# Optimization experiments

Hardware: AMD Instinct MI355X
Metric: run time of the kernel (lower is better)

## Reference

```python
import jax, jax.numpy as jnp
import numpy as np
from math import ceil, sqrt

# Inner module: Linear(2048,4096)+ReLU, Linear(4096,4096)+ReLU, Linear(4096,2048)
D_IN, D_H, D_OUT = 2048, 4096, 2048
BATCH = 4096
# named_modules() order: each Linear yields weight then bias; ReLU skipped
SHAPES = [(D_H, D_IN), (D_H,), (D_H, D_H), (D_H,), (D_OUT, D_H), (D_OUT,)]
NUM_P = sum(int(np.prod(s)) for s in SHAPES)  # 33_566_720
SIZE_N = ceil(sqrt(NUM_P))                    # 5794
SIZE_M = ceil(1.0 * SIZE_N / 2)               # 2897 (compress = 1.0)


def setup_inputs() -> dict:
    key = jax.random.key(0)
    k1, k2, k3 = jax.random.split(key, 3)
    k = sqrt(12) / 2 * SIZE_M ** (-0.25)  # norm_V init bound
    V1 = jax.random.uniform(k1, (SIZE_N, SIZE_M), jnp.float32, -k, k)
    V2 = jax.random.uniform(k2, (SIZE_M, SIZE_N), jnp.float32, -k, k)
    x = jax.random.normal(k3, (BATCH, D_IN), jnp.float32)
    return {"x": x, "V1": V1, "V2": V2}


def _unpack(Vf):
    # scatter-copy: contiguous slices of flattened V -> weights/biases in traversal order
    params, i = [], 0
    for s in SHAPES:
        n = int(np.prod(s))
        params.append(Vf[i:i + n].reshape(s))
        i += n
    return params


def reference(x, V1, V2):
    # WandBtoV: low-rank reconstruction then per-element copy into weights (fused here)
    Vf = (V1 @ V2).reshape(-1)  # [SIZE_N*SIZE_N]; only first NUM_P elements used
    W1, b1, W2, b2, W3, b3 = _unpack(Vf)
    h = jax.nn.relu(x @ W1.T + b1)   # [B, D_H]
    h = jax.nn.relu(h @ W2.T + b2)   # [B, D_H]
    return h @ W3.T + b3             # [B, D_OUT]
```

## Files before the change

kernel.cpp:

```cpp
#include <hip/hip_runtime.h>
#include <stdint.h>

typedef __attribute__((ext_vector_type(8)))  __bf16 bf16x8;
typedef __attribute__((ext_vector_type(16))) float  f32x16;
typedef unsigned short u16;
typedef __attribute__((ext_vector_type(8))) unsigned short u16x8;

#define GLOBAL_AS __attribute__((address_space(1)))
#define LDS_AS    __attribute__((address_space(3)))

__device__ __forceinline__ void load_lds16(const void* g, void* l) {
    __builtin_amdgcn_global_load_lds((const GLOBAL_AS void*)g, (LDS_AS void*)l, 16, 0, 0);
}

__device__ __forceinline__ u16 f2bf(float f) {
    union { float f; uint32_t u; } v; v.f = f;
    uint32_t r = v.u + 0x7FFFu + ((v.u >> 16) & 1u);
    return (u16)(r >> 16);
}
__device__ __forceinline__ float b2f(u16 b) {
    union { uint32_t u; float f; } v; v.u = ((uint32_t)b) << 16;
    return v.f;
}

__global__ void k_conv_pad(const float* __restrict__ in, u16* __restrict__ out,
                           int rIn, int cIn, int cOut, int total8) {
    int idx = blockIdx.x * blockDim.x + threadIdx.x;
    if (idx >= total8) return;
    int c8n = cOut >> 3;
    int r  = idx / c8n;
    int c0 = (idx - r * c8n) << 3;
    u16x8 o;
#pragma unroll
    for (int j = 0; j < 8; ++j) {
        int c = c0 + j;
        o[j] = (r < rIn && c < cIn) ? f2bf(in[(size_t)r * cIn + c]) : (u16)0;
    }
    *(u16x8*)(out + (size_t)r * cOut + c0) = o;
}

__global__ void k_transpose_conv(const float* __restrict__ in, u16* __restrict__ out,
                                 int kIn, int nIn, int kOut) {
    __shared__ float tile[32][33];
    int k0 = blockIdx.x * 32, n0 = blockIdx.y * 32;
    int tx = threadIdx.x, ty = threadIdx.y;
#pragma unroll
    for (int i = 0; i < 4; ++i) {
        int k = k0 + ty + i * 8, n = n0 + tx;
        tile[ty + i * 8][tx] = (k < kIn && n < nIn) ? in[(size_t)k * nIn + n] : 0.f;
    }
    __syncthreads();
#pragma unroll
    for (int i = 0; i < 4; ++i) {
        int n = n0 + ty + i * 8, k = k0 + tx;
        out[(size_t)n * kOut + k] = f2bf(tile[tx][ty + i * 8]);
    }
}

template <int MODE>
__global__ __launch_bounds__(256, 4) void k_gemm_bt(
    const u16* __restrict__ A, const u16* __restrict__ B,
    const u16* __restrict__ bias, void* __restrict__ Cv,
    int K, int ldc, int mReal, int nReal) {
    (void)bias;
    __shared__ __align__(16) char lds[32768];
    char* As = lds;
    char* Bs = lds + 16384;

    const int tid  = threadIdx.x;
    const int w    = tid >> 6, lane = tid & 63;
    const int l31  = lane & 31, hi = lane >> 5;
    const int wm   = (w & 1) * 64, wn = (w >> 1) * 64;
    const int bm   = blockIdx.y * 128, bn = blockIdx.x * 128;

    const int srcRow = tid >> 3;
    const int srcCol = (tid & 7) ^ (srcRow & 7);
    const u16* aSrc = A + (size_t)(bm + srcRow) * K + (srcCol << 3);
    const u16* bSrc = B + (size_t)(bn + srcRow) * K + (srcCol << 3);
    char* aDst = As + ((tid & ~63) << 4);
    char* bDst = Bs + ((tid & ~63) << 4);

    const int aRow0 = (wm + l31) * 128;
    const int aRow1 = (wm + 32 + l31) * 128;
    const int bRow0 = (wn + l31) * 128;
    const int bRow1 = (wn + 32 + l31) * 128;

    f32x16 acc[2][2];
#pragma unroll
    for (int i = 0; i < 2; ++i)
#pragma unroll
        for (int j = 0; j < 2; ++j) acc[i][j] = (f32x16)(0.f);

    for (int k0 = 0; k0 < K; k0 += 64) {
#pragma unroll
        for (int t = 0; t < 4; ++t) {
            load_lds16(aSrc + (size_t)(t * 32) * K, aDst + t * 4096);
            load_lds16(bSrc + (size_t)(t * 32) * K, bDst + t * 4096);
        }
        aSrc += 64; bSrc += 64;
        __syncthreads();
#pragma unroll
        for (int ks = 0; ks < 4; ++ks) {
            const int swz = (((ks * 2 + hi) ^ (l31 & 7)) << 4);
            bf16x8 af[2], bfr[2];
            af[0]  = *(const bf16x8*)(As + aRow0 + swz);
            af[1]  = *(const bf16x8*)(As + aRow1 + swz);
            bfr[0] = *(const bf16x8*)(Bs + bRow0 + swz);
            bfr[1] = *(const bf16x8*)(Bs + bRow1 + swz);
#pragma unroll
            for (int mi = 0; mi < 2; ++mi)
#pragma unroll
                for (int ni = 0; ni < 2; ++ni)
                    acc[mi][ni] = __builtin_amdgcn_mfma_f32_32x32x16_bf16(
                        af[mi], bfr[ni], acc[mi][ni], 0, 0, 0);
        }
        __syncthreads();
    }

    float bv[2];
    if (MODE >= 1) {
#pragma unroll
        for (int ni = 0; ni < 2; ++ni) bv[ni] = b2f(bias[bn + wn + ni * 32 + l31]);
    }
#pragma unroll
    for (int mi = 0; mi < 2; ++mi) {
#pragma unroll
        for (int reg = 0; reg < 16; ++reg) {
            int row = bm + wm + mi * 32 + (reg & 3) + 8 * (reg >> 2) + 4 * hi;
#pragma unroll
            for (int ni = 0; ni < 2; ++ni) {
                int col = bn + wn + ni * 32 + l31;
                float v = acc[mi][ni][reg];
                if (MODE == 0) {
                    if (row < mReal && col < nReal)
                        ((u16*)Cv)[(size_t)row * ldc + col] = f2bf(v);
                } else if (MODE == 1) {
                    v += bv[ni];
                    v = v > 0.f ? v : 0.f;
                    ((u16*)Cv)[(size_t)row * ldc + col] = f2bf(v);
                } else {
                    ((float*)Cv)[(size_t)row * ldc + col] = v + bv[ni];
                }
            }
        }
    }
}


#define BARRIER() do { asm volatile("" ::: "memory"); \
                       __builtin_amdgcn_s_barrier(); \
                       asm volatile("" ::: "memory"); } while (0)
#define LGKM0()   do { asm volatile("s_waitcnt lgkmcnt(0)" ::: "memory"); \
                       __builtin_amdgcn_sched_barrier(0); } while (0)
#define VMCNT0()  do { asm volatile("s_waitcnt vmcnt(0)" ::: "memory"); \
                       __builtin_amdgcn_sched_barrier(0); } while (0)

#define STAGE8(bb, koff) do { \
    _Pragma("unroll") for (int t = 0; t < 4; ++t) \
        load_lds16(aS + (koff) + (size_t)(t * 64) * K, (bb) + wOff + t * 8192); \
    _Pragma("unroll") for (int t = 0; t < 4; ++t) \
        load_lds16(bS + (koff) + (size_t)(t * 64) * K, (bb) + 32768 + wOff + t * 8192); \
} while (0)

#define RD6(bb, p, FA, FB) do { \
    FA[0] = *(const bf16x8*)((bb) + aB +     0 + (p) * 1024); \
    FA[1] = *(const bf16x8*)((bb) + aB +  4096 + (p) * 1024); \
    FA[2] = *(const bf16x8*)((bb) + aB +  8192 + (p) * 1024); \
    FA[3] = *(const bf16x8*)((bb) + aB + 12288 + (p) * 1024); \
    FB[0] = *(const bf16x8*)((bb) + bB +     0 + (p) * 1024); \
    FB[1] = *(const bf16x8*)((bb) + bB +  4096 + (p) * 1024); \
} while (0)

#define MM8(FA, FB) do { \
    __builtin_amdgcn_s_setprio(1); \
    acc[0][0] = __builtin_amdgcn_mfma_f32_32x32x16_bf16(FA[0], FB[0], acc[0][0], 0, 0, 0); \
    acc[1][0] = __builtin_amdgcn_mfma_f32_32x32x16_bf16(FA[1], FB[0], acc[1][0], 0, 0, 0); \
    acc[2][0] = __builtin_amdgcn_mfma_f32_32x32x16_bf16(FA[2], FB[0], acc[2][0], 0, 0, 0); \
    acc[3][0] = __builtin_amdgcn_mfma_f32_32x32x16_bf16(FA[3], FB[0], acc[3][0], 0, 0, 0); \
    acc[0][1] = __builtin_amdgcn_mfma_f32_32x32x16_bf16(FA[0], FB[1], acc[0][1], 0, 0, 0); \
    acc[1][1] = __builtin_amdgcn_mfma_f32_32x32x16_bf16(FA[1], FB[1], acc[1][1], 0, 0, 0); \
    acc[2][1] = __builtin_amdgcn_mfma_f32_32x32x16_bf16(FA[2], FB[1], acc[2][1], 0, 0, 0); \
    acc[3][1] = __builtin_amdgcn_mfma_f32_32x32x16_bf16(FA[3], FB[1], acc[3][1], 0, 0, 0); \
    __builtin_amdgcn_s_setprio(0); \
} while (0)

template <int MODE>
__global__ __launch_bounds__(512, 2) void k_gemm256(
    const u16* __restrict__ A, const u16* __restrict__ B,
    const u16* __restrict__ bias, void* __restrict__ Cv,
    int K, int ldc, int mReal, int nReal, int gx, int nTiles) {
    __shared__ __align__(16) char lds[131072];

    const int tid  = threadIdx.x;
    const int w    = tid >> 6, lane = tid & 63;
    const int l31  = lane & 31, hi = lane >> 5;
    const int wr   = w & 1, wc = w >> 1;

    const int cpx = (int)gridDim.x >> 3;
    const int wg0 = ((int)blockIdx.x & 7) * cpx + ((int)blockIdx.x >> 3);

    char* const buf0 = lds;
    char* const buf1 = lds + 65536;

    const int srcRowT = ((w >> 2) * 32) + l31;
    const int kOffT   = (w & 3) * 16 + (hi << 3);
    const int wOff    = w * 1024;

    const int aB = wr * 16384 + lane * 16;
    const int bB = 32768 + wc * 8192 + lane * 16;

    const int nIt = K >> 7;

    for (int v = wg0; v < nTiles; v += (int)gridDim.x) {
        const int bm = (v / gx) * 256;
        const int bn = (v % gx) * 256;
        const u16* const aS = A + (size_t)(bm + srcRowT) * K + kOffT;
        const u16* const bS = B + (size_t)(bn + srcRowT) * K + kOffT;

        f32x16 acc[4][2];
#pragma unroll
        for (int i = 0; i < 4; ++i)
#pragma unroll
            for (int j = 0; j < 2; ++j) acc[i][j] = (f32x16)(0.f);

        bf16x8 xa[4], xb[2], ya[4], yb[2];

        STAGE8(buf0, 0);
        VMCNT0();
        BARRIER();

        size_t ko = 0;
#pragma unroll 1
        for (int it = 0; it < nIt; ++it) {
            STAGE8(buf1, ko + 64);
            RD6(buf0, 0, xa, xb);
            RD6(buf0, 1, ya, yb);
            MM8(xa, xb);
            RD6(buf0, 2, xa, xb);
            MM8(ya, yb);
            RD6(buf0, 3, ya, yb);
            MM8(xa, xb);
            LGKM0(); VMCNT0(); BARRIER();
            if (it + 1 < nIt) { STAGE8(buf0, ko + 128); }
            MM8(ya, yb);
            RD6(buf1, 0, xa, xb);
            RD6(buf1, 1, ya, yb);
            MM8(xa, xb);
            RD6(buf1, 2, xa, xb);
            MM8(ya, yb);
            RD6(buf1, 3, ya, yb);
            MM8(xa, xb);
            LGKM0(); VMCNT0(); BARRIER();
            MM8(ya, yb);
            ko += 128;
        }

        float bv[2];
        if (MODE >= 1) {
#pragma unroll
            for (int ni = 0; ni < 2; ++ni) bv[ni] = b2f(bias[bn + wc * 64 + ni * 32 + l31]);
        }
#pragma unroll
        for (int mi = 0; mi < 4; ++mi) {
#pragma unroll
            for (int reg = 0; reg < 16; ++reg) {
                const int row = bm + wr * 128 + mi * 32 + (reg & 3) + 8 * (reg >> 2) + 4 * hi;
#pragma unroll
                for (int ni = 0; ni < 2; ++ni) {
                    const int col = bn + wc * 64 + ni * 32 + l31;
                    float vv = acc[mi][ni][reg];
                    if (MODE == 0) {
                        if (row < mReal && col < nReal)
                            ((u16*)Cv)[(size_t)row * ldc + col] = f2bf(vv);
                    } else if (MODE == 1) {
                        vv += bv[ni];
                        vv = vv > 0.f ? vv : 0.f;
                        ((u16*)Cv)[(size_t)row * ldc + col] = f2bf(vv);
                    } else {
                        ((float*)Cv)[(size_t)row * ldc + col] = vv + bv[ni];
                    }
                }
            }
        }
    }
}

extern "C" void kernel_launch(void* const* d_in, const int* in_sizes, int n_in,
                              void* d_out, int out_size, void* d_ws, size_t ws_size,
                              hipStream_t stream) {
    (void)in_sizes; (void)n_in; (void)out_size; (void)ws_size;
    const float* x  = (const float*)d_in[0];
    const float* V1 = (const float*)d_in[1];
    const float* V2 = (const float*)d_in[2];

    char* ws = (char*)d_ws;
    u16* Vf   = (u16*)(ws);
    u16* V1b  = (u16*)(ws + 67141120);
    u16* V2bT = (u16*)(ws + 67141120 + 34668544);
    u16* Xb   = (u16*)(ws + 67141120 + 2 * 34668544);
    u16* H1   = V1b;
    u16* H2   = V2bT;

    k_conv_pad<<<8464, 256, 0, stream>>>(V1, V1b, 5794, 2897, 2944, 5888 * 2944 / 8);
    k_transpose_conv<<<dim3(92, 184), dim3(32, 8), 0, stream>>>(V2, V2bT, 2897, 5794, 2944);
    k_conv_pad<<<4096, 256, 0, stream>>>(x, Xb, 4096, 2048, 2048, 4096 * 2048 / 8);

    k_gemm256<0><<<512, 512, 0, stream>>>(V1b, V2bT, nullptr, Vf,
                                          2944, 5794, 5794, 5794, 23, 529);
    k_gemm256<1><<<256, 512, 0, stream>>>(Xb, Vf + 0, Vf + 8388608, H1,
                                          2048, 4096, 4096, 4096, 16, 256);
    k_gemm256<1><<<256, 512, 0, stream>>>(H1, Vf + 8392704, Vf + 25169920, H2,
                                          4096, 4096, 4096, 4096, 16, 256);
    k_gemm_bt<2><<<dim3(16, 32), 256, 0, stream>>>(H2, Vf + 25174016, Vf + 33562624, d_out,
                                                   4096, 2048, 4096, 2048);
}
```

Baseline: 852.9 us.

## Replace 256x256 persistent GEMM with 256x128 non-persistent tiles and swizzled LDS

The 512-thread persistent 256x256-tile GEMM is replaced by a 256-thread kernel computing 256x128 tiles, one tile per workgroup, with a K-step of 64 and a smaller double-buffered LDS footprint. LDS rows are stored with an XOR swizzle on 16-byte chunks to avoid bank conflicts. Block-to-XCD remapping now handles grid sizes that are not a multiple of 8. The aim is more workgroups, better occupancy and fewer LDS conflicts, at the cost of less operand reuse per tile and more global traffic.

```diff
diff --git a/kernel.cpp b/kernel.cpp
--- a/kernel.cpp
+++ b/kernel.cpp
@@ -155,20 +155,21 @@
 #define VMCNT0()  do { asm volatile("s_waitcnt vmcnt(0)" ::: "memory"); \
                        __builtin_amdgcn_sched_barrier(0); } while (0)
 
-#define STAGE8(bb, koff) do { \
+#define STAGE6(bb, koff) do { \
     _Pragma("unroll") for (int t = 0; t < 4; ++t) \
-        load_lds16(aS + (koff) + (size_t)(t * 64) * K, (bb) + wOff + t * 8192); \
-    _Pragma("unroll") for (int t = 0; t < 4; ++t) \
-        load_lds16(bS + (koff) + (size_t)(t * 64) * K, (bb) + 32768 + wOff + t * 8192); \
+        load_lds16(aS + (koff) + (size_t)(t * 64) * K, (bb) + t * 4096 + wOff); \
+    _Pragma("unroll") for (int t = 0; t < 2; ++t) \
+        load_lds16(bS + (koff) + (size_t)(t * 64) * K, (bb) + 16384 + t * 4096 + wOff); \
 } while (0)
 
 #define RD6(bb, p, FA, FB) do { \
-    FA[0] = *(const bf16x8*)((bb) + aB +     0 + (p) * 1024); \
-    FA[1] = *(const bf16x8*)((bb) + aB +  4096 + (p) * 1024); \
-    FA[2] = *(const bf16x8*)((bb) + aB +  8192 + (p) * 1024); \
-    FA[3] = *(const bf16x8*)((bb) + aB + 12288 + (p) * 1024); \
-    FB[0] = *(const bf16x8*)((bb) + bB +     0 + (p) * 1024); \
-    FB[1] = *(const bf16x8*)((bb) + bB +  4096 + (p) * 1024); \
+    const int co_ = ch0 ^ ((p) << 5); \
+    FA[0] = *(const bf16x8*)((bb) + aR +    0 + co_); \
+    FA[1] = *(const bf16x8*)((bb) + aR + 2048 + co_); \
+    FA[2] = *(const bf16x8*)((bb) + aR + 4096 + co_); \
+    FA[3] = *(const bf16x8*)((bb) + aR + 6144 + co_); \
+    FB[0] = *(const bf16x8*)((bb) + bR +    0 + co_); \
+    FB[1] = *(const bf16x8*)((bb) + bR + 2048 + co_); \
 } while (0)
 
 #define MM8(FA, FB) do { \
@@ -185,100 +186,92 @@
 } while (0)
 
 template <int MODE>
-__global__ __launch_bounds__(512, 2) void k_gemm256(
+__global__ __launch_bounds__(256, 2) void k_gemm128(
     const u16* __restrict__ A, const u16* __restrict__ B,
     const u16* __restrict__ bias, void* __restrict__ Cv,
-    int K, int ldc, int mReal, int nReal, int gx, int nTiles) {
-    __shared__ __align__(16) char lds[131072];
+    int K, int ldc, int mReal, int nReal, int gx) {
+    __shared__ __align__(16) char lds[49152];
 
     const int tid  = threadIdx.x;
     const int w    = tid >> 6, lane = tid & 63;
     const int l31  = lane & 31, hi = lane >> 5;
     const int wr   = w & 1, wc = w >> 1;
 
-    const int cpx = (int)gridDim.x >> 3;
-    const int wg0 = ((int)blockIdx.x & 7) * cpx + ((int)blockIdx.x >> 3);
+    const int nwg = (int)gridDim.x;
+    const int q   = nwg >> 3, r = nwg & 7;
+    const int xcd = (int)blockIdx.x & 7, lid = (int)blockIdx.x >> 3;
+    const int wg  = (xcd < r ? xcd * (q + 1) : r * (q + 1) + (xcd - r) * q) + lid;
+    const int bm  = (wg / gx) * 256;
+    const int bn  = (wg % gx) * 128;
 
     char* const buf0 = lds;
-    char* const buf1 = lds + 65536;
-
-    const int srcRowT = ((w >> 2) * 32) + l31;
-    const int kOffT   = (w & 3) * 16 + (hi << 3);
-    const int wOff    = w * 1024;
-
-    const int aB = wr * 16384 + lane * 16;
-    const int bB = 32768 + wc * 8192 + lane * 16;
-
-    const int nIt = K >> 7;
-
-    for (int v = wg0; v < nTiles; v += (int)gridDim.x) {
-        const int bm = (v / gx) * 256;
-        const int bn = (v % gx) * 256;
-        const u16* const aS = A + (size_t)(bm + srcRowT) * K + kOffT;
-        const u16* const bS = B + (size_t)(bn + srcRowT) * K + kOffT;
-
-        f32x16 acc[4][2];
-#pragma unroll
-        for (int i = 0; i < 4; ++i)
-#pragma unroll
-            for (int j = 0; j < 2; ++j) acc[i][j] = (f32x16)(0.f);
-
-        bf16x8 xa[4], xb[2], ya[4], yb[2];
-
-        STAGE8(buf0, 0);
-        VMCNT0();
-        BARRIER();
-
-        size_t ko = 0;
+    char* const buf1 = lds + 24576;
+
+    const int srcRow = tid >> 2;
+    const int srcCh  = (tid & 3) ^ ((srcRow >> 1) & 3);
+    const int wOff   = (tid & ~63) << 4;
+
+    const int aR  = (wr * 128 + l31) * 64;
+    const int bR  = 16384 + (wc * 64 + l31) * 64;
+    const int ch0 = ((hi ^ ((l31 >> 1) & 3))) << 4;
+
+    const u16* const aS = A + (size_t)(bm + srcRow) * K + (srcCh << 3);
+    const u16* const bS = B + (size_t)(bn + srcRow) * K + (srcCh << 3);
+
+    f32x16 acc[4][2];
+#pragma unroll
+    for (int i = 0; i < 4; ++i)
+#pragma unroll
+        for (int j = 0; j < 2; ++j) acc[i][j] = (f32x16)(0.f);
+
+    bf16x8 xa[4], xb[2], ya[4], yb[2];
+
+    STAGE6(buf0, 0);
+    VMCNT0();
+    BARRIER();
+
+    const int nIt = K >> 6;
+    size_t ko = 0;
 #pragma unroll 1
-        for (int it = 0; it < nIt; ++it) {
-            STAGE8(buf1, ko + 64);
-            RD6(buf0, 0, xa, xb);
-            RD6(buf0, 1, ya, yb);
-            MM8(xa, xb);
-            RD6(buf0, 2, xa, xb);
-            MM8(ya, yb);
-            RD6(buf0, 3, ya, yb);
-            MM8(xa, xb);
-            LGKM0(); VMCNT0(); BARRIER();
-            if (it + 1 < nIt) { STAGE8(buf0, ko + 128); }
-            MM8(ya, yb);
-            RD6(buf1, 0, xa, xb);
-            RD6(buf1, 1, ya, yb);
-            MM8(xa, xb);
-            RD6(buf1, 2, xa, xb);
-            MM8(ya, yb);
-            RD6(buf1, 3, ya, yb);
-            MM8(xa, xb);
-            LGKM0(); VMCNT0(); BARRIER();
-            MM8(ya, yb);
-            ko += 128;
-        }
-
-        float bv[2];
-        if (MODE >= 1) {
-#pragma unroll
-            for (int ni = 0; ni < 2; ++ni) bv[ni] = b2f(bias[bn + wc * 64 + ni * 32 + l31]);
-        }
-#pragma unroll
-        for (int mi = 0; mi < 4; ++mi) {
-#pragma unroll
-            for (int reg = 0; reg < 16; ++reg) {
-                const int row = bm + wr * 128 + mi * 32 + (reg & 3) + 8 * (reg >> 2) + 4 * hi;
-#pragma unroll
-                for (int ni = 0; ni < 2; ++ni) {
-                    const int col = bn + wc * 64 + ni * 32 + l31;
-                    float vv = acc[mi][ni][reg];
-                    if (MODE == 0) {
-                        if (row < mReal && col < nReal)
-                            ((u16*)Cv)[(size_t)row * ldc + col] = f2bf(vv);
-                    } else if (MODE == 1) {
-                        vv += bv[ni];
-                        vv = vv > 0.f ? vv : 0.f;
+    for (int it = 0; it < nIt; ++it) {
+        STAGE6(buf1, ko + 32);
+        RD6(buf0, 0, xa, xb);
+        RD6(buf0, 1, ya, yb);
+        MM8(xa, xb);
+        LGKM0(); VMCNT0(); BARRIER();
+        if (it + 1 < nIt) { STAGE6(buf0, ko + 64); }
+        MM8(ya, yb);
+        RD6(buf1, 0, xa, xb);
+        RD6(buf1, 1, ya, yb);
+        MM8(xa, xb);
+        LGKM0(); VMCNT0(); BARRIER();
+        MM8(ya, yb);
+        ko += 64;
+    }
+
+    float bv[2];
+    if (MODE >= 1) {
+#pragma unroll
+        for (int ni = 0; ni < 2; ++ni) bv[ni] = b2f(bias[bn + wc * 64 + ni * 32 + l31]);
+    }
+#pragma unroll
+    for (int mi = 0; mi < 4; ++mi) {
+#pragma unroll
+        for (int reg = 0; reg < 16; ++reg) {
+            const int row = bm + wr * 128 + mi * 32 + (reg & 3) + 8 * (reg >> 2) + 4 * hi;
+#pragma unroll
+            for (int ni = 0; ni < 2; ++ni) {
+                const int col = bn + wc * 64 + ni * 32 + l31;
+                float vv = acc[mi][ni][reg];
+                if (MODE == 0) {
+                    if (row < mReal && col < nReal)
                         ((u16*)Cv)[(size_t)row * ldc + col] = f2bf(vv);
-                    } else {
-                        ((float*)Cv)[(size_t)row * ldc + col] = vv + bv[ni];
-                    }
+                } else if (MODE == 1) {
+                    vv += bv[ni];
+                    vv = vv > 0.f ? vv : 0.f;
+                    ((u16*)Cv)[(size_t)row * ldc + col] = f2bf(vv);
+                } else {
+                    ((float*)Cv)[(size_t)row * ldc + col] = vv + bv[ni];
                 }
             }
         }
@@ -305,12 +298,12 @@
     k_transpose_conv<<<dim3(92, 184), dim3(32, 8), 0, stream>>>(V2, V2bT, 2897, 5794, 2944);
     k_conv_pad<<<4096, 256, 0, stream>>>(x, Xb, 4096, 2048, 2048, 4096 * 2048 / 8);
 
-    k_gemm256<0><<<512, 512, 0, stream>>>(V1b, V2bT, nullptr, Vf,
-                                          2944, 5794, 5794, 5794, 23, 529);
-    k_gemm256<1><<<256, 512, 0, stream>>>(Xb, Vf + 0, Vf + 8388608, H1,
-                                          2048, 4096, 4096, 4096, 16, 256);
-    k_gemm256<1><<<256, 512, 0, stream>>>(H1, Vf + 8392704, Vf + 25169920, H2,
-                                          4096, 4096, 4096, 4096, 16, 256);
+    k_gemm128<0><<<1058, 256, 0, stream>>>(V1b, V2bT, nullptr, Vf,
+                                           2944, 5794, 5794, 5794, 46);
+    k_gemm128<1><<<512, 256, 0, stream>>>(Xb, Vf + 0, Vf + 8388608, H1,
+                                          2048, 4096, 4096, 4096, 32);
+    k_gemm128<1><<<512, 256, 0, stream>>>(H1, Vf + 8392704, Vf + 25169920, H2,
+                                          4096, 4096, 4096, 4096, 32);
     k_gemm_bt<2><<<dim3(16, 32), 256, 0, stream>>>(H2, Vf + 25174016, Vf + 33562624, d_out,
                                                    4096, 2048, 4096, 2048);
 }
```

Result: faster. 752.6 us (-11.8%).
